# Kernel tuning notes

Measured on AMD Instinct MI355X. Metric: run time of the kernel, lower is better.

## Reference

```python
import jax, jax.numpy as jnp
import numpy as np

HIDDEN = 128
N_NODES = 100000
N_EDGES = 200000
NEG_SLOPE = 0.01  # torch LeakyReLU default


def setup_inputs() -> dict:
    key = jax.random.key(0)
    ks = jax.random.split(key, 12)
    h = HIDDEN
    lim = 1.0 / np.sqrt(h)
    lim3 = 1.0 / np.sqrt(3 * h)
    u = lambda k, shape, l: jax.random.uniform(k, shape, jnp.float32, -l, l)
    return {
        "x_src": jax.random.normal(ks[0], (N_NODES, h), jnp.float32),
        "x_dst": jax.random.normal(ks[1], (N_NODES, h), jnp.float32),
        "edge_index": jax.random.randint(ks[2], (2, N_EDGES), 0, N_NODES, jnp.int64),
        # parent_encoder Linear(h, h)
        "Wp": u(ks[3], (h, h), lim), "bp": u(ks[4], (h,), lim),
        # child_encoder Linear(h, h)
        "Wc": u(ks[5], (h, h), lim), "bc": u(ks[6], (h,), lim),
        # edge_weight_mlp: Linear(3h, h) -> ReLU -> Linear(h, h)
        "W1": u(ks[7], (h, 3 * h), lim3), "b1": u(ks[8], (h,), lim3),
        "W2": u(ks[9], (h, h), lim), "b2": u(ks[10], (h,), lim),
    }


def reference(x_src, x_dst, edge_index, Wp, bp, Wc, bc, W1, b1, W2, b2):
    # gather node feats per edge  [E, h]
    par = x_src[edge_index[0]]
    cld = x_dst[edge_index[1]]
    # dual encoders: Linear + LeakyReLU (Dropout is identity in eval)
    enc_p = jax.nn.leaky_relu(par @ Wp.T + bp, NEG_SLOPE)
    enc_c = jax.nn.leaky_relu(cld @ Wc.T + bc, NEG_SLOPE)
    diff = jnp.abs(par - cld)
    ef = jnp.concatenate([enc_p, enc_c, diff], axis=-1)  # [E, 3h]
    # edge_weight_mlp
    edge_attr = jax.nn.relu(ef @ W1.T + b1) @ W2.T + b2  # [E, h]
    return edge_attr
```

## Files before the change

### kernel.cpp

```cpp
#include <hip/hip_runtime.h>

typedef unsigned short u16;
typedef __attribute__((ext_vector_type(8))) short v8s;
typedef __attribute__((ext_vector_type(4))) float v4f;
typedef __attribute__((ext_vector_type(4))) float f4;

#define HID 128
#define TM  64
#define EFS 392
#define HS  136
#define FOS 136

__device__ __forceinline__ u16 f2b(float f) {
    union { float f; unsigned u; } v; v.f = f;
    unsigned u = v.u;
    u += 0x7fffu + ((u >> 16) & 1u);
    return (u16)(u >> 16);
}

#define MFMA(A, B, C) __builtin_amdgcn_mfma_f32_16x16x32_bf16(A, B, C, 0, 0, 0)

__global__ void cvt_weights(const float* __restrict__ Wp, const float* __restrict__ Wc,
                            const float* __restrict__ W1, const float* __restrict__ W2,
                            u16* __restrict__ dst)
{
    int i = blockIdx.x * 256 + threadIdx.x;
    const float* s; int off;
    if (i < 4096)       { s = Wp; off = 0; }
    else if (i < 8192)  { s = Wc; off = 4096; }
    else if (i < 20480) { s = W1; off = 8192; }
    else                { s = W2; off = 20480; }
    int j = i - off;
    f4 v = ((const f4*)s)[j];
    u16* d = dst + (size_t)i * 4;
    d[0] = f2b(v[0]); d[1] = f2b(v[1]); d[2] = f2b(v[2]); d[3] = f2b(v[3]);
}

__global__ __launch_bounds__(256, 2) void edge_attr_kernel(
    const float* __restrict__ x_src, const float* __restrict__ x_dst,
    const int* __restrict__ ei,
    const u16* __restrict__ wsW,
    const float* __restrict__ bp, const float* __restrict__ bc,
    const float* __restrict__ b1, const float* __restrict__ b2,
    float* __restrict__ out, int E)
{
    __shared__ __align__(16) u16 sEF[TM * EFS];
    __shared__ __align__(16) u16 sH [TM * HS];

    const u16* wsWp = wsW;
    const u16* wsWc = wsW + 16384;
    const u16* wsW1 = wsW + 32768;
    const u16* wsW2 = wsW + 81920;

    const int t  = threadIdx.x;
    const int e0 = blockIdx.x * TM;
    const int* ei0 = ei;
    const int* ei1 = ei + E;

    #pragma unroll
    for (int i = 0; i < 4; ++i) {
        int idx = t + i * 256;
        int r = idx >> 4;
        int c = (idx & 15) << 3;
        int e = e0 + r; if (e >= E) e = E - 1;
        const f4* ps = (const f4*)(x_src + (size_t)ei0[e] * HID + c);
        const f4* qs = (const f4*)(x_dst + (size_t)ei1[e] * HID + c);
        f4 p0 = ps[0], p1 = ps[1];
        f4 q0 = qs[0], q1 = qs[1];
        v8s pb, qb, db;
        #pragma unroll
        for (int j = 0; j < 4; ++j) {
            pb[j]     = (short)f2b(p0[j]);
            pb[j + 4] = (short)f2b(p1[j]);
            qb[j]     = (short)f2b(q0[j]);
            qb[j + 4] = (short)f2b(q1[j]);
            db[j]     = (short)f2b(fabsf(p0[j] - q0[j]));
            db[j + 4] = (short)f2b(fabsf(p1[j] - q1[j]));
        }
        *(v8s*)&sEF[r * EFS       + c] = pb;
        *(v8s*)&sEF[r * EFS + 128 + c] = qb;
        *(v8s*)&sEF[r * EFS + 256 + c] = db;
    }
    __syncthreads();

    const int lane = t & 63;
    const int ln = lane & 15;
    const int lq = lane >> 4;
    const int n0 = (t >> 6) * 32;

    {
        v8s Bp[2][4], Bc[2][4];
        float bpv[2], bcv[2];
        #pragma unroll
        for (int nt = 0; nt < 2; ++nt) {
            int n = n0 + nt * 16 + ln;
            bpv[nt] = bp[n];
            bcv[nt] = bc[n];
            #pragma unroll
            for (int kt = 0; kt < 4; ++kt) {
                Bp[nt][kt] = *(const v8s*)(wsWp + (size_t)n * HID + kt * 32 + lq * 8);
                Bc[nt][kt] = *(const v8s*)(wsWc + (size_t)n * HID + kt * 32 + lq * 8);
            }
        }
        v4f aP[4][2], aC[4][2];
        #pragma unroll
        for (int mt = 0; mt < 4; ++mt)
            #pragma unroll
            for (int nt = 0; nt < 2; ++nt) {
                aP[mt][nt] = (v4f){0.f, 0.f, 0.f, 0.f};
                aC[mt][nt] = (v4f){0.f, 0.f, 0.f, 0.f};
            }
        #pragma unroll
        for (int mt = 0; mt < 4; ++mt) {
            const int rbase = (mt * 16 + ln) * EFS + lq * 8;
            v8s A[4];
            #pragma unroll
            for (int kt = 0; kt < 4; ++kt) A[kt] = *(const v8s*)&sEF[rbase + kt * 32];
            #pragma unroll
            for (int nt = 0; nt < 2; ++nt)
                #pragma unroll
                for (int kt = 0; kt < 4; ++kt) aP[mt][nt] = MFMA(A[kt], Bp[nt][kt], aP[mt][nt]);
            #pragma unroll
            for (int kt = 0; kt < 4; ++kt) A[kt] = *(const v8s*)&sEF[rbase + 128 + kt * 32];
            #pragma unroll
            for (int nt = 0; nt < 2; ++nt)
                #pragma unroll
                for (int kt = 0; kt < 4; ++kt) aC[mt][nt] = MFMA(A[kt], Bc[nt][kt], aC[mt][nt]);
        }
        __syncthreads();
        #pragma unroll
        for (int mt = 0; mt < 4; ++mt)
            #pragma unroll
            for (int nt = 0; nt < 2; ++nt)
                #pragma unroll
                for (int rg = 0; rg < 4; ++rg) {
                    int row = mt * 16 + lq * 4 + rg;
                    int col = n0 + nt * 16 + ln;
                    float vp = aP[mt][nt][rg] + bpv[nt];
                    vp = vp > 0.f ? vp : 0.01f * vp;
                    sEF[row * EFS + col] = f2b(vp);
                    float vc = aC[mt][nt][rg] + bcv[nt];
                    vc = vc > 0.f ? vc : 0.01f * vc;
                    sEF[row * EFS + 128 + col] = f2b(vc);
                }
        __syncthreads();
    }

    {
        float b1v[2];
        #pragma unroll
        for (int nt = 0; nt < 2; ++nt) b1v[nt] = b1[n0 + nt * 16 + ln];
        v4f acc[4][2];
        #pragma unroll
        for (int mt = 0; mt < 4; ++mt)
            #pragma unroll
            for (int nt = 0; nt < 2; ++nt) acc[mt][nt] = (v4f){0.f, 0.f, 0.f, 0.f};
        #pragma unroll
        for (int ktc = 0; ktc < 3; ++ktc) {
            v8s B[2][4];
            #pragma unroll
            for (int nt = 0; nt < 2; ++nt) {
                int n = n0 + nt * 16 + ln;
                #pragma unroll
                for (int k4 = 0; k4 < 4; ++k4)
                    B[nt][k4] = *(const v8s*)(wsW1 + (size_t)n * 384 + ktc * 128 + k4 * 32 + lq * 8);
            }
            #pragma unroll
            for (int mt = 0; mt < 4; ++mt) {
                const int rbase = (mt * 16 + ln) * EFS + ktc * 128 + lq * 8;
                v8s A[4];
                #pragma unroll
                for (int k4 = 0; k4 < 4; ++k4) A[k4] = *(const v8s*)&sEF[rbase + k4 * 32];
                #pragma unroll
                for (int nt = 0; nt < 2; ++nt)
                    #pragma unroll
                    for (int k4 = 0; k4 < 4; ++k4) acc[mt][nt] = MFMA(A[k4], B[nt][k4], acc[mt][nt]);
            }
        }
        #pragma unroll
        for (int mt = 0; mt < 4; ++mt)
            #pragma unroll
            for (int nt = 0; nt < 2; ++nt)
                #pragma unroll
                for (int rg = 0; rg < 4; ++rg) {
                    int row = mt * 16 + lq * 4 + rg;
                    int col = n0 + nt * 16 + ln;
                    float v = acc[mt][nt][rg] + b1v[nt];
                    sH[row * HS + col] = f2b(fmaxf(v, 0.f));
                }
        __syncthreads();
    }

    {
        float* sF = (float*)sEF;
        v8s B2[2][4];
        float b2v[2];
        #pragma unroll
        for (int nt = 0; nt < 2; ++nt) {
            int n = n0 + nt * 16 + ln;
            b2v[nt] = b2[n];
            #pragma unroll
            for (int kt = 0; kt < 4; ++kt)
                B2[nt][kt] = *(const v8s*)(wsW2 + (size_t)n * HID + kt * 32 + lq * 8);
        }
        v4f acc[4][2];
        #pragma unroll
        for (int mt = 0; mt < 4; ++mt)
            #pragma unroll
            for (int nt = 0; nt < 2; ++nt) acc[mt][nt] = (v4f){0.f, 0.f, 0.f, 0.f};
        #pragma unroll
        for (int mt = 0; mt < 4; ++mt) {
            const int rbase = (mt * 16 + ln) * HS + lq * 8;
            v8s A[4];
            #pragma unroll
            for (int kt = 0; kt < 4; ++kt) A[kt] = *(const v8s*)&sH[rbase + kt * 32];
            #pragma unroll
            for (int nt = 0; nt < 2; ++nt)
                #pragma unroll
                for (int kt = 0; kt < 4; ++kt) acc[mt][nt] = MFMA(A[kt], B2[nt][kt], acc[mt][nt]);
        }
        #pragma unroll
        for (int mt = 0; mt < 4; ++mt)
            #pragma unroll
            for (int nt = 0; nt < 2; ++nt)
                #pragma unroll
                for (int rg = 0; rg < 4; ++rg) {
                    int row = mt * 16 + lq * 4 + rg;
                    int col = n0 + nt * 16 + ln;
                    sF[row * FOS + col] = acc[mt][nt][rg] + b2v[nt];
                }
        __syncthreads();
    }

    {
        const float* sF = (const float*)sEF;
        #pragma unroll
        for (int i = 0; i < 8; ++i) {
            int idx = t + i * 256;
            int r = idx >> 5;
            int c = (idx & 31) << 2;
            int e = e0 + r;
            if (e < E)
                *(f4*)(out + (size_t)e * HID + c) = *(const f4*)&sF[r * FOS + c];
        }
    }
}

extern "C" void kernel_launch(void* const* d_in, const int* in_sizes, int n_in,
                              void* d_out, int out_size, void* d_ws, size_t ws_size,
                              hipStream_t stream) {
    const float* x_src = (const float*)d_in[0];
    const float* x_dst = (const float*)d_in[1];
    const int*   ei    = (const int*)d_in[2];
    const float* Wp    = (const float*)d_in[3];
    const float* bp    = (const float*)d_in[4];
    const float* Wc    = (const float*)d_in[5];
    const float* bc    = (const float*)d_in[6];
    const float* W1    = (const float*)d_in[7];
    const float* b1    = (const float*)d_in[8];
    const float* W2    = (const float*)d_in[9];
    const float* b2    = (const float*)d_in[10];
    float* out = (float*)d_out;
    u16* wsW = (u16*)d_ws;

    int E = in_sizes[2] / 2;

    cvt_weights<<<96, 256, 0, stream>>>(Wp, Wc, W1, W2, wsW);

    int blocks = (E + TM - 1) / TM;
    edge_attr_kernel<<<blocks, 256, 0, stream>>>(
        x_src, x_dst, ei, wsW, bp, bc, b1, b2, out, E);
}
```

Baseline: 285.6 us.

## Use 512-thread blocks with 2x4 warp tiling and drop the separate hidden buffer

```diff
diff --git a/kernel.cpp b/kernel.cpp
--- a/kernel.cpp
+++ b/kernel.cpp
@@ -8,8 +8,7 @@
 #define HID 128
 #define TM  64
 #define EFS 392
-#define HS  136
-#define FOS 136
+#define FOS 132
 
 __device__ __forceinline__ u16 f2b(float f) {
     union { float f; unsigned u; } v; v.f = f;
@@ -36,7 +35,7 @@
     d[0] = f2b(v[0]); d[1] = f2b(v[1]); d[2] = f2b(v[2]); d[3] = f2b(v[3]);
 }
 
-__global__ __launch_bounds__(256, 2) void edge_attr_kernel(
+__global__ __launch_bounds__(512, 6) void edge_attr_kernel(
     const float* __restrict__ x_src, const float* __restrict__ x_dst,
     const int* __restrict__ ei,
     const u16* __restrict__ wsW,
@@ -45,7 +44,6 @@
     float* __restrict__ out, int E)
 {
     __shared__ __align__(16) u16 sEF[TM * EFS];
-    __shared__ __align__(16) u16 sH [TM * HS];
 
     const u16* wsWp = wsW;
     const u16* wsWc = wsW + 16384;
@@ -58,8 +56,8 @@
     const int* ei1 = ei + E;
 
     #pragma unroll
-    for (int i = 0; i < 4; ++i) {
-        int idx = t + i * 256;
+    for (int i = 0; i < 2; ++i) {
+        int idx = t + i * 512;
         int r = idx >> 4;
         int c = (idx & 15) << 3;
         int e = e0 + r; if (e >= E) e = E - 1;
@@ -86,73 +84,83 @@
     const int lane = t & 63;
     const int ln = lane & 15;
     const int lq = lane >> 4;
-    const int n0 = (t >> 6) * 32;
-
-    {
-        v8s Bp[2][4], Bc[2][4];
-        float bpv[2], bcv[2];
+    const int w  = t >> 6;
+    const int r0 = (w >> 2) * 32;
+    const int c0 = (w & 3) * 32;
+
+    v4f aP[2][2], aC[2][2];
+    float bpv[2], bcv[2];
+    #pragma unroll
+    for (int nt = 0; nt < 2; ++nt) {
+        bpv[nt] = bp[c0 + nt * 16 + ln];
+        bcv[nt] = bc[c0 + nt * 16 + ln];
+    }
+    {
+        v8s B[2][4];
         #pragma unroll
         for (int nt = 0; nt < 2; ++nt) {
-            int n = n0 + nt * 16 + ln;
-            bpv[nt] = bp[n];
-            bcv[nt] = bc[n];
-            #pragma unroll
-            for (int kt = 0; kt < 4; ++kt) {
-                Bp[nt][kt] = *(const v8s*)(wsWp + (size_t)n * HID + kt * 32 + lq * 8);
-                Bc[nt][kt] = *(const v8s*)(wsWc + (size_t)n * HID + kt * 32 + lq * 8);
-            }
-        }
-        v4f aP[4][2], aC[4][2];
-        #pragma unroll
-        for (int mt = 0; mt < 4; ++mt)
+            int n = c0 + nt * 16 + ln;
+            #pragma unroll
+            for (int kt = 0; kt < 4; ++kt)
+                B[nt][kt] = *(const v8s*)(wsWp + (size_t)n * HID + kt * 32 + lq * 8);
+        }
+        #pragma unroll
+        for (int mt = 0; mt < 2; ++mt) {
+            const int rb = (r0 + mt * 16 + ln) * EFS + lq * 8;
+            v8s A[4];
+            #pragma unroll
+            for (int kt = 0; kt < 4; ++kt) A[kt] = *(const v8s*)&sEF[rb + kt * 32];
             #pragma unroll
             for (int nt = 0; nt < 2; ++nt) {
                 aP[mt][nt] = (v4f){0.f, 0.f, 0.f, 0.f};
-                aC[mt][nt] = (v4f){0.f, 0.f, 0.f, 0.f};
-            }
-        #pragma unroll
-        for (int mt = 0; mt < 4; ++mt) {
-            const int rbase = (mt * 16 + ln) * EFS + lq * 8;
+                #pragma unroll
+                for (int kt = 0; kt < 4; ++kt) aP[mt][nt] = MFMA(A[kt], B[nt][kt], aP[mt][nt]);
+            }
+        }
+    }
+    #pragma unroll
+    for (int nt = 0; nt < 2; ++nt) {
+        v8s B[4];
+        int n = c0 + nt * 16 + ln;
+        #pragma unroll
+        for (int kt = 0; kt < 4; ++kt)
+            B[kt] = *(const v8s*)(wsWc + (size_t)n * HID + kt * 32 + lq * 8);
+        #pragma unroll
+        for (int mt = 0; mt < 2; ++mt) {
+            const int rb = (r0 + mt * 16 + ln) * EFS + 128 + lq * 8;
             v8s A[4];
             #pragma unroll
-            for (int kt = 0; kt < 4; ++kt) A[kt] = *(const v8s*)&sEF[rbase + kt * 32];
-            #pragma unroll
-            for (int nt = 0; nt < 2; ++nt)
-                #pragma unroll
-                for (int kt = 0; kt < 4; ++kt) aP[mt][nt] = MFMA(A[kt], Bp[nt][kt], aP[mt][nt]);
-            #pragma unroll
-            for (int kt = 0; kt < 4; ++kt) A[kt] = *(const v8s*)&sEF[rbase + 128 + kt * 32];
-            #pragma unroll
-            for (int nt = 0; nt < 2; ++nt)
-                #pragma unroll
-                for (int kt = 0; kt < 4; ++kt) aC[mt][nt] = MFMA(A[kt], Bc[nt][kt], aC[mt][nt]);
-        }
-        __syncthreads();
-        #pragma unroll
-        for (int mt = 0; mt < 4; ++mt)
-            #pragma unroll
-            for (int nt = 0; nt < 2; ++nt)
-                #pragma unroll
-                for (int rg = 0; rg < 4; ++rg) {
-                    int row = mt * 16 + lq * 4 + rg;
-                    int col = n0 + nt * 16 + ln;
-                    float vp = aP[mt][nt][rg] + bpv[nt];
-                    vp = vp > 0.f ? vp : 0.01f * vp;
-                    sEF[row * EFS + col] = f2b(vp);
-                    float vc = aC[mt][nt][rg] + bcv[nt];
-                    vc = vc > 0.f ? vc : 0.01f * vc;
-                    sEF[row * EFS + 128 + col] = f2b(vc);
-                }
-        __syncthreads();
-    }
+            for (int kt = 0; kt < 4; ++kt) A[kt] = *(const v8s*)&sEF[rb + kt * 32];
+            aC[mt][nt] = (v4f){0.f, 0.f, 0.f, 0.f};
+            #pragma unroll
+            for (int kt = 0; kt < 4; ++kt) aC[mt][nt] = MFMA(A[kt], B[kt], aC[mt][nt]);
+        }
+    }
+    __syncthreads();
+    #pragma unroll
+    for (int mt = 0; mt < 2; ++mt)
+        #pragma unroll
+        for (int nt = 0; nt < 2; ++nt)
+            #pragma unroll
+            for (int rg = 0; rg < 4; ++rg) {
+                int row = r0 + mt * 16 + lq * 4 + rg;
+                int col = c0 + nt * 16 + ln;
+                float vp = aP[mt][nt][rg] + bpv[nt];
+                vp = vp > 0.f ? vp : 0.01f * vp;
+                sEF[row * EFS + col] = f2b(vp);
+                float vc = aC[mt][nt][rg] + bcv[nt];
+                vc = vc > 0.f ? vc : 0.01f * vc;
+                sEF[row * EFS + 128 + col] = f2b(vc);
+            }
+    __syncthreads();
 
     {
         float b1v[2];
         #pragma unroll
-        for (int nt = 0; nt < 2; ++nt) b1v[nt] = b1[n0 + nt * 16 + ln];
-        v4f acc[4][2];
-        #pragma unroll
-        for (int mt = 0; mt < 4; ++mt)
+        for (int nt = 0; nt < 2; ++nt) b1v[nt] = b1[c0 + nt * 16 + ln];
+        v4f acc[2][2];
+        #pragma unroll
+        for (int mt = 0; mt < 2; ++mt)
             #pragma unroll
             for (int nt = 0; nt < 2; ++nt) acc[mt][nt] = (v4f){0.f, 0.f, 0.f, 0.f};
         #pragma unroll
@@ -160,73 +168,74 @@
             v8s B[2][4];
             #pragma unroll
             for (int nt = 0; nt < 2; ++nt) {
-                int n = n0 + nt * 16 + ln;
+                int n = c0 + nt * 16 + ln;
                 #pragma unroll
                 for (int k4 = 0; k4 < 4; ++k4)
                     B[nt][k4] = *(const v8s*)(wsW1 + (size_t)n * 384 + ktc * 128 + k4 * 32 + lq * 8);
             }
             #pragma unroll
-            for (int mt = 0; mt < 4; ++mt) {
-                const int rbase = (mt * 16 + ln) * EFS + ktc * 128 + lq * 8;
+            for (int mt = 0; mt < 2; ++mt) {
+                const int rb = (r0 + mt * 16 + ln) * EFS + ktc * 128 + lq * 8;
                 v8s A[4];
                 #pragma unroll
-                for (int k4 = 0; k4 < 4; ++k4) A[k4] = *(const v8s*)&sEF[rbase + k4 * 32];
+                for (int k4 = 0; k4 < 4; ++k4) A[k4] = *(const v8s*)&sEF[rb + k4 * 32];
                 #pragma unroll
                 for (int nt = 0; nt < 2; ++nt)
                     #pragma unroll
                     for (int k4 = 0; k4 < 4; ++k4) acc[mt][nt] = MFMA(A[k4], B[nt][k4], acc[mt][nt]);
             }
         }
-        #pragma unroll
-        for (int mt = 0; mt < 4; ++mt)
+        __syncthreads();
+        #pragma unroll
+        for (int mt = 0; mt < 2; ++mt)
             #pragma unroll
             for (int nt = 0; nt < 2; ++nt)
                 #pragma unroll
                 for (int rg = 0; rg < 4; ++rg) {
-                    int row = mt * 16 + lq * 4 + rg;
-                    int col = n0 + nt * 16 + ln;
+                    int row = r0 + mt * 16 + lq * 4 + rg;
+                    int col = c0 + nt * 16 + ln;
                     float v = acc[mt][nt][rg] + b1v[nt];
-                    sH[row * HS + col] = f2b(fmaxf(v, 0.f));
+                    sEF[row * EFS + 256 + col] = f2b(fmaxf(v, 0.f));
                 }
         __syncthreads();
     }
 
     {
+        float b2v[2];
+        #pragma unroll
+        for (int nt = 0; nt < 2; ++nt) b2v[nt] = b2[c0 + nt * 16 + ln];
+        v4f acc[2][2];
+        v8s B[2][4];
+        #pragma unroll
+        for (int nt = 0; nt < 2; ++nt) {
+            int n = c0 + nt * 16 + ln;
+            #pragma unroll
+            for (int kt = 0; kt < 4; ++kt)
+                B[nt][kt] = *(const v8s*)(wsW2 + (size_t)n * HID + kt * 32 + lq * 8);
+        }
+        #pragma unroll
+        for (int mt = 0; mt < 2; ++mt) {
+            const int rb = (r0 + mt * 16 + ln) * EFS + 256 + lq * 8;
+            v8s A[4];
+            #pragma unroll
+            for (int kt = 0; kt < 4; ++kt) A[kt] = *(const v8s*)&sEF[rb + kt * 32];
+            #pragma unroll
+            for (int nt = 0; nt < 2; ++nt) {
+                acc[mt][nt] = (v4f){0.f, 0.f, 0.f, 0.f};
+                #pragma unroll
+                for (int kt = 0; kt < 4; ++kt) acc[mt][nt] = MFMA(A[kt], B[nt][kt], acc[mt][nt]);
+            }
+        }
+        __syncthreads();
         float* sF = (float*)sEF;
-        v8s B2[2][4];
-        float b2v[2];
-        #pragma unroll
-        for (int nt = 0; nt < 2; ++nt) {
-            int n = n0 + nt * 16 + ln;
-            b2v[nt] = b2[n];
-            #pragma unroll
-            for (int kt = 0; kt < 4; ++kt)
-                B2[nt][kt] = *(const v8s*)(wsW2 + (size_t)n * HID + kt * 32 + lq * 8);
-        }
-        v4f acc[4][2];
-        #pragma unroll
-        for (int mt = 0; mt < 4; ++mt)
-            #pragma unroll
-            for (int nt = 0; nt < 2; ++nt) acc[mt][nt] = (v4f){0.f, 0.f, 0.f, 0.f};
-        #pragma unroll
-        for (int mt = 0; mt < 4; ++mt) {
-            const int rbase = (mt * 16 + ln) * HS + lq * 8;
-            v8s A[4];
-            #pragma unroll
-            for (int kt = 0; kt < 4; ++kt) A[kt] = *(const v8s*)&sH[rbase + kt * 32];
+        #pragma unroll
+        for (int mt = 0; mt < 2; ++mt)
             #pragma unroll
             for (int nt = 0; nt < 2; ++nt)
                 #pragma unroll
-                for (int kt = 0; kt < 4; ++kt) acc[mt][nt] = MFMA(A[kt], B2[nt][kt], acc[mt][nt]);
-        }
-        #pragma unroll
-        for (int mt = 0; mt < 4; ++mt)
-            #pragma unroll
-            for (int nt = 0; nt < 2; ++nt)
-                #pragma unroll
                 for (int rg = 0; rg < 4; ++rg) {
-                    int row = mt * 16 + lq * 4 + rg;
-                    int col = n0 + nt * 16 + ln;
+                    int row = r0 + mt * 16 + lq * 4 + rg;
+                    int col = c0 + nt * 16 + ln;
                     sF[row * FOS + col] = acc[mt][nt][rg] + b2v[nt];
                 }
         __syncthreads();
@@ -235,8 +244,8 @@
     {
         const float* sF = (const float*)sEF;
         #pragma unroll
-        for (int i = 0; i < 8; ++i) {
-            int idx = t + i * 256;
+        for (int i = 0; i < 4; ++i) {
+            int idx = t + i * 512;
             int r = idx >> 5;
             int c = (idx & 31) << 2;
             int e = e0 + r;
@@ -268,6 +277,6 @@
     cvt_weights<<<96, 256, 0, stream>>>(Wp, Wc, W1, W2, wsW);
 
     int blocks = (E + TM - 1) / TM;
-    edge_attr_kernel<<<blocks, 256, 0, stream>>>(
+    edge_attr_kernel<<<blocks, 512, 0, stream>>>(
         x_src, x_dst, ei, wsW, bp, bc, b1, b2, out, E);
 }
```

New measurement: 332.8 us. +16.5%, slower.

## Reuse edge-feature LDS for hidden layer and store output directly to raise occupancy

Applied to the files above, without the earlier changes.

```diff
diff --git a/kernel.cpp b/kernel.cpp
--- a/kernel.cpp
+++ b/kernel.cpp
@@ -8,8 +8,6 @@
 #define HID 128
 #define TM  64
 #define EFS 392
-#define HS  136
-#define FOS 136
 
 __device__ __forceinline__ u16 f2b(float f) {
     union { float f; unsigned u; } v; v.f = f;
@@ -36,7 +34,7 @@
     d[0] = f2b(v[0]); d[1] = f2b(v[1]); d[2] = f2b(v[2]); d[3] = f2b(v[3]);
 }
 
-__global__ __launch_bounds__(256, 2) void edge_attr_kernel(
+__global__ __launch_bounds__(256, 3) void edge_attr_kernel(
     const float* __restrict__ x_src, const float* __restrict__ x_dst,
     const int* __restrict__ ei,
     const u16* __restrict__ wsW,
@@ -45,7 +43,6 @@
     float* __restrict__ out, int E)
 {
     __shared__ __align__(16) u16 sEF[TM * EFS];
-    __shared__ __align__(16) u16 sH [TM * HS];
 
     const u16* wsWp = wsW;
     const u16* wsWc = wsW + 16384;
@@ -57,29 +54,42 @@
     const int* ei0 = ei;
     const int* ei1 = ei + E;
 
-    #pragma unroll
-    for (int i = 0; i < 4; ++i) {
-        int idx = t + i * 256;
-        int r = idx >> 4;
-        int c = (idx & 15) << 3;
-        int e = e0 + r; if (e >= E) e = E - 1;
-        const f4* ps = (const f4*)(x_src + (size_t)ei0[e] * HID + c);
-        const f4* qs = (const f4*)(x_dst + (size_t)ei1[e] * HID + c);
-        f4 p0 = ps[0], p1 = ps[1];
-        f4 q0 = qs[0], q1 = qs[1];
-        v8s pb, qb, db;
-        #pragma unroll
-        for (int j = 0; j < 4; ++j) {
-            pb[j]     = (short)f2b(p0[j]);
-            pb[j + 4] = (short)f2b(p1[j]);
-            qb[j]     = (short)f2b(q0[j]);
-            qb[j + 4] = (short)f2b(q1[j]);
-            db[j]     = (short)f2b(fabsf(p0[j] - q0[j]));
-            db[j + 4] = (short)f2b(fabsf(p1[j] - q1[j]));
-        }
-        *(v8s*)&sEF[r * EFS       + c] = pb;
-        *(v8s*)&sEF[r * EFS + 128 + c] = qb;
-        *(v8s*)&sEF[r * EFS + 256 + c] = db;
+    {
+        const int gr = t >> 4;
+        const int gc = (t & 15) << 3;
+
+        int ia[4], ib[4];
+        #pragma unroll
+        for (int i = 0; i < 4; ++i) {
+            int e = e0 + gr + i * 16; if (e >= E) e = E - 1;
+            ia[i] = ei0[e]; ib[i] = ei1[e];
+        }
+        f4 P[4][2], Q[4][2];
+        #pragma unroll
+        for (int i = 0; i < 4; ++i) {
+            const f4* ps = (const f4*)(x_src + (size_t)ia[i] * HID + gc);
+            const f4* qs = (const f4*)(x_dst + (size_t)ib[i] * HID + gc);
+            P[i][0] = ps[0]; P[i][1] = ps[1];
+            Q[i][0] = qs[0]; Q[i][1] = qs[1];
+        }
+        #pragma unroll
+        for (int i = 0; i < 4; ++i) {
+            int r = gr + i * 16;
+            f4 p0 = P[i][0], p1 = P[i][1], q0 = Q[i][0], q1 = Q[i][1];
+            v8s pb, qb, db;
+            #pragma unroll
+            for (int j = 0; j < 4; ++j) {
+                pb[j]     = (short)f2b(p0[j]);
+                pb[j + 4] = (short)f2b(p1[j]);
+                qb[j]     = (short)f2b(q0[j]);
+                qb[j + 4] = (short)f2b(q1[j]);
+                db[j]     = (short)f2b(fabsf(p0[j] - q0[j]));
+                db[j + 4] = (short)f2b(fabsf(p1[j] - q1[j]));
+            }
+            *(v8s*)&sEF[r * EFS       + gc] = pb;
+            *(v8s*)&sEF[r * EFS + 128 + gc] = qb;
+            *(v8s*)&sEF[r * EFS + 256 + gc] = db;
+        }
     }
     __syncthreads();
 
@@ -177,6 +187,7 @@
                     for (int k4 = 0; k4 < 4; ++k4) acc[mt][nt] = MFMA(A[k4], B[nt][k4], acc[mt][nt]);
             }
         }
+        __syncthreads();
         #pragma unroll
         for (int mt = 0; mt < 4; ++mt)
             #pragma unroll
@@ -186,15 +197,14 @@
                     int row = mt * 16 + lq * 4 + rg;
                     int col = n0 + nt * 16 + ln;
                     float v = acc[mt][nt][rg] + b1v[nt];
-                    sH[row * HS + col] = f2b(fmaxf(v, 0.f));
+                    sEF[row * EFS + 256 + col] = f2b(fmaxf(v, 0.f));
                 }
         __syncthreads();
     }
 
     {
-        float* sF = (float*)sEF;
+        float b2v[2];
         v8s B2[2][4];
-        float b2v[2];
         #pragma unroll
         for (int nt = 0; nt < 2; ++nt) {
             int n = n0 + nt * 16 + ln;
@@ -203,45 +213,29 @@
             for (int kt = 0; kt < 4; ++kt)
                 B2[nt][kt] = *(const v8s*)(wsW2 + (size_t)n * HID + kt * 32 + lq * 8);
         }
-        v4f acc[4][2];
-        #pragma unroll
-        for (int mt = 0; mt < 4; ++mt)
-            #pragma unroll
-            for (int nt = 0; nt < 2; ++nt) acc[mt][nt] = (v4f){0.f, 0.f, 0.f, 0.f};
         #pragma unroll
         for (int mt = 0; mt < 4; ++mt) {
-            const int rbase = (mt * 16 + ln) * HS + lq * 8;
+            const int rbase = (mt * 16 + ln) * EFS + 256 + lq * 8;
             v8s A[4];
             #pragma unroll
-            for (int kt = 0; kt < 4; ++kt) A[kt] = *(const v8s*)&sH[rbase + kt * 32];
-            #pragma unroll
-            for (int nt = 0; nt < 2; ++nt)
-                #pragma unroll
-                for (int kt = 0; kt < 4; ++kt) acc[mt][nt] = MFMA(A[kt], B2[nt][kt], acc[mt][nt]);
-        }
-        #pragma unroll
-        for (int mt = 0; mt < 4; ++mt)
+            for (int kt = 0; kt < 4; ++kt) A[kt] = *(const v8s*)&sEF[rbase + kt * 32];
+            v4f acc[2];
+            #pragma unroll
+            for (int nt = 0; nt < 2; ++nt) {
+                acc[nt] = (v4f){0.f, 0.f, 0.f, 0.f};
+                #pragma unroll
+                for (int kt = 0; kt < 4; ++kt) acc[nt] = MFMA(A[kt], B2[nt][kt], acc[nt]);
+            }
             #pragma unroll
             for (int nt = 0; nt < 2; ++nt)
                 #pragma unroll
                 for (int rg = 0; rg < 4; ++rg) {
                     int row = mt * 16 + lq * 4 + rg;
                     int col = n0 + nt * 16 + ln;
-                    sF[row * FOS + col] = acc[mt][nt][rg] + b2v[nt];
+                    int e = e0 + row;
+                    if (e < E)
+                        out[(size_t)e * HID + col] = acc[nt][rg] + b2v[nt];
                 }
-        __syncthreads();
-    }
-
-    {
-        const float* sF = (const float*)sEF;
-        #pragma unroll
-        for (int i = 0; i < 8; ++i) {
-            int idx = t + i * 256;
-            int r = idx >> 5;
-            int c = (idx & 31) << 2;
-            int e = e0 + r;
-            if (e < E)
-                *(f4*)(out + (size_t)e * HID + c) = *(const f4*)&sF[r * FOS + c];
         }
     }
 }
```

Measured after the change: 291.4 us. 1.02x slower.
